# Kernel optimization log

Measured on AMD Instinct MI355X. Metric: run time of the kernel, lower is better.

Reference implementation:

```python
import jax, jax.numpy as jnp
import numpy as np

QMAX = 7.0  # 4-bit symmetric: levels in [-8, 7]

def quant4(w):
    # per-tensor symmetric 4-bit fake-quant with straight-through estimator
    s = jnp.max(jnp.abs(w)) / QMAX
    q = jnp.clip(jnp.round(w / s), -8.0, 7.0) * s
    return w + jax.lax.stop_gradient(q - w)

def setup_inputs() -> dict:
    key = jax.random.key(0)
    ks = jax.random.split(key, 7)
    B = 2048
    x = jax.random.normal(ks[0], (B, 1, 31, 16, 31), dtype=jnp.float32)
    # conv: out_ch=1, in_ch=1, kernel (5,3,5)
    w_conv = jax.random.normal(ks[1], (1, 1, 5, 3, 5), dtype=jnp.float32) * 0.1
    b_conv = jax.random.normal(ks[2], (1,), dtype=jnp.float32) * 0.1
    w_fc1 = jax.random.normal(ks[3], (128, 343), dtype=jnp.float32) * 0.05
    b_fc1 = jax.random.normal(ks[4], (128,), dtype=jnp.float32) * 0.05
    w_fc2 = jax.random.normal(ks[5], (4, 128), dtype=jnp.float32) * 0.05
    b_fc2 = jax.random.normal(ks[6], (4,), dtype=jnp.float32) * 0.05
    return {"x": x, "w_conv": w_conv, "b_conv": b_conv,
            "w_fc1": w_fc1, "b_fc1": b_fc1, "w_fc2": w_fc2, "b_fc2": b_fc2}

def reference(x, w_conv, b_conv, w_fc1, b_fc1, w_fc2, b_fc2):
    # QuantConv3d: 4-bit quantized weights, stride (2,1,2), no padding
    c1 = jax.lax.conv_general_dilated(
        x, quant4(w_conv), window_strides=(2, 1, 2), padding='VALID',
        dimension_numbers=('NCDHW', 'OIDHW', 'NCDHW'))
    c1 = c1 + b_conv.reshape(1, -1, 1, 1, 1)          # [B,1,14,14,14]
    # MaxPool3d(2)
    p1 = jax.lax.reduce_window(c1, -jnp.inf, jax.lax.max,
                               (1, 1, 2, 2, 2), (1, 1, 2, 2, 2), 'VALID')  # [B,1,7,7,7]
    f = p1.reshape(p1.shape[0], -1)                   # [B,343]
    a1 = jax.nn.relu(f @ quant4(w_fc1).T + b_fc1)     # [B,128]
    s2 = a1 @ quant4(w_fc2).T + b_fc2                 # [B,4]
    return jax.nn.softmax(s2, axis=1)
```

## Files before the change

kernel.cpp:

```cpp
#include <hip/hip_runtime.h>

#define WS_WCONV   128
#define WS_W1T     256
#define WS_W2      44160

__device__ __forceinline__ float q4(float w, float s) {
  if (s <= 0.f) return 0.f;
  float r = rintf(w / s);
  r = fminf(fmaxf(r, -8.f), 7.f);
  return r * s;
}

__global__ __launch_bounds__(256) void quant_all(
    const float* __restrict__ wconv, const float* __restrict__ w1,
    const float* __restrict__ w2, float* __restrict__ ws) {
  __shared__ float red[256];
  int b = blockIdx.x, t = threadIdx.x;
  if (b < 88) {
    const float4* w4 = (const float4*)w1;
    float m = 0.f;
    for (int i = t; i < 10976; i += 256) {
      float4 v = w4[i];
      m = fmaxf(m, fmaxf(fmaxf(fabsf(v.x), fabsf(v.y)),
                         fmaxf(fabsf(v.z), fabsf(v.w))));
    }
    red[t] = m;
    __syncthreads();
    for (int s = 128; s > 0; s >>= 1) {
      if (t < s) red[t] = fmaxf(red[t], red[t + s]);
      __syncthreads();
    }
    float s = red[0] * (1.0f / 7.0f);
    #pragma unroll
    for (int k = 0; k < 2; ++k) {
      int idx = b * 512 + k * 256 + t;
      if (idx < 43904) {
        float q = q4(w1[idx], s);
        int o = idx / 343;
        int j = idx - o * 343;
        ws[WS_W1T + j * 128 + o] = q;
      }
    }
  } else {
    float mc = (t < 75) ? fabsf(wconv[t]) : 0.f;
    float m2 = 0.f;
    for (int i = t; i < 512; i += 256) m2 = fmaxf(m2, fabsf(w2[i]));
    red[t] = mc;
    __syncthreads();
    for (int s = 128; s > 0; s >>= 1) {
      if (t < s) red[t] = fmaxf(red[t], red[t + s]);
      __syncthreads();
    }
    float sc = red[0] * (1.0f / 7.0f);
    __syncthreads();
    red[t] = m2;
    __syncthreads();
    for (int s = 128; s > 0; s >>= 1) {
      if (t < s) red[t] = fmaxf(red[t], red[t + s]);
      __syncthreads();
    }
    float s2 = red[0] * (1.0f / 7.0f);
    if (t < 75) ws[WS_WCONV + t] = q4(wconv[t], sc);
    #pragma unroll
    for (int k = 0; k < 2; ++k) {
      int idx = k * 256 + t;
      ws[WS_W2 + idx] = q4(w2[idx], s2);
    }
  }
}

struct __align__(4) f4u { float x, y, z, w; };

__device__ __forceinline__ void conv_global(
    const float* __restrict__ xb, const float* __restrict__ wq,
    int t, float bc, float* __restrict__ feat) {
  if (t >= 343) return;
  int pdl = t / 49;
  int rr  = t - pdl * 49;
  int ph  = rr / 7;
  int pw  = rr - ph * 7;
  float c[2][2][2];
  #pragma unroll
  for (int i = 0; i < 8; ++i) ((float*)c)[i] = 0.f;
  const float* b0 = xb + pdl * 1984 + ph * 62 + pw * 4;
  #pragma unroll
  for (int dd = 0; dd < 7; ++dd) {
    const float* rb = b0 + dd * 496;
    #pragma unroll
    for (int hh = 0; hh < 4; ++hh) {
      const float* rp = rb + hh * 31;
      f4u A = *(const f4u*)rp;
      f4u B = *(const f4u*)(rp + 3);
      float row[7] = {A.x, A.y, A.z, A.w, B.y, B.z, B.w};
      #pragma unroll
      for (int odp = 0; odp < 2; ++odp) {
        int kd = dd - 2 * odp;
        if (kd < 0 || kd > 4) continue;
        #pragma unroll
        for (int ohp = 0; ohp < 2; ++ohp) {
          int kh = hh - ohp;
          if (kh < 0 || kh > 2) continue;
          #pragma unroll
          for (int owp = 0; owp < 2; ++owp) {
            float a = c[odp][ohp][owp];
            #pragma unroll
            for (int kw = 0; kw < 5; ++kw)
              a = fmaf(row[2 * owp + kw], wq[kd * 15 + kh * 5 + kw], a);
            c[odp][ohp][owp] = a;
          }
        }
      }
    }
  }
  float m = ((float*)c)[0];
  #pragma unroll
  for (int i = 1; i < 8; ++i) m = fmaxf(m, ((float*)c)[i]);
  feat[pdl * 49 + rr] = m + bc;
}

__global__ __launch_bounds__(384, 6) void fused_net(
    const float* __restrict__ x, const float* __restrict__ bconv,
    const float* __restrict__ ws, const float* __restrict__ bfc1,
    const float* __restrict__ bfc2, float* __restrict__ out) {
  __shared__ alignas(16) float feat[344];
  __shared__ alignas(16) float fc1p[128];
  __shared__ alignas(16) float a1[128];
  __shared__ float s2[4];
  int t = threadIdx.x;
  int b = blockIdx.x;
  const float* wq = ws + WS_WCONV;
  float bc = bconv[0];
  const float* xb = x + (size_t)b * 15376;

  if (t == 383) feat[343] = 0.f;
  conv_global(xb, wq, t, bc, feat);
  __syncthreads();

  int g = (t >> 7) & 1, o = t & 127;
  float acc = 0.f;
  if (t < 256) {
    const float* w1T = ws + WS_W1T;
    int j0 = g ? 172 : 0;
    const float4* f4 = (const float4*)&feat[j0];
    const float* wp = w1T + j0 * 128 + o;
    float q0 = 0.f, q1 = 0.f, q2 = 0.f, q3 = 0.f;
    for (int q = 0; q < 43; ++q) {
      float4 ff = f4[q];
      q0 = fmaf(ff.x, wp[0],   q0);
      q1 = fmaf(ff.y, wp[128], q1);
      q2 = fmaf(ff.z, wp[256], q2);
      q3 = fmaf(ff.w, wp[384], q3);
      wp += 512;
    }
    acc = (q0 + q1) + (q2 + q3);
    if (g) fc1p[o] = acc;
  }
  __syncthreads();
  if (t < 256 && !g) a1[o] = fmaxf(acc + fc1p[o] + bfc1[o], 0.f);
  __syncthreads();

  if (t < 64) {
    int cls = t & 3, kk = t >> 2;
    const float* w2p = ws + WS_W2 + cls * 128 + kk * 8;
    const float* av = a1 + kk * 8;
    float p = 0.f;
    #pragma unroll
    for (int i = 0; i < 8; ++i) p = fmaf(av[i], w2p[i], p);
    p += __shfl_down(p, 32);
    p += __shfl_down(p, 16);
    p += __shfl_down(p, 8);
    p += __shfl_down(p, 4);
    if (t < 4) s2[t] = p + bfc2[t];
  }
  __syncthreads();
  if (t < 4) {
    float v0 = s2[0], v1 = s2[1], v2 = s2[2], v3 = s2[3];
    float m = fmaxf(fmaxf(v0, v1), fmaxf(v2, v3));
    float e0 = expf(v0 - m), e1 = expf(v1 - m);
    float e2 = expf(v2 - m), e3 = expf(v3 - m);
    float inv = 1.f / (e0 + e1 + e2 + e3);
    float mine = (t == 0) ? e0 : (t == 1) ? e1 : (t == 2) ? e2 : e3;
    out[b * 4 + t] = mine * inv;
  }
}

extern "C" void kernel_launch(void* const* d_in, const int* in_sizes, int n_in,
                              void* d_out, int out_size, void* d_ws, size_t ws_size,
                              hipStream_t stream) {
  const float* x     = (const float*)d_in[0];
  const float* wconv = (const float*)d_in[1];
  const float* bconv = (const float*)d_in[2];
  const float* wfc1  = (const float*)d_in[3];
  const float* bfc1  = (const float*)d_in[4];
  const float* wfc2  = (const float*)d_in[5];
  const float* bfc2  = (const float*)d_in[6];
  float* out = (float*)d_out;
  float* ws  = (float*)d_ws;

  quant_all<<<89, 256, 0, stream>>>(wconv, wfc1, wfc2, ws);
  fused_net<<<2048, 384, 0, stream>>>(x, bconv, ws, bfc1, bfc2, out);
}
```

Measured before the change: 243.4 us.

## Split fused net into dense conv-pool kernel and batched FC kernel

Splits the single fused per-sample kernel into a conv+pool kernel that maps every pooled output across all batches onto fully occupied 256-thread blocks, and an FC kernel that handles four samples per block so each fc1 weight load is reused across four samples. Pooled features go through a workspace buffer in global memory. This removes the idle threads of the 384-thread blocks (only 343 did conv work) and amortizes weight reads. In exchange it adds a global round-trip for features and an extra kernel launch.

```diff
diff --git a/kernel.cpp b/kernel.cpp
--- a/kernel.cpp
+++ b/kernel.cpp
@@ -3,6 +3,7 @@
 #define WS_WCONV   128
 #define WS_W1T     256
 #define WS_W2      44160
+#define WS_FEAT    45056
 
 __device__ __forceinline__ float q4(float w, float s) {
   if (s <= 0.f) return 0.f;
@@ -71,14 +72,19 @@
 
 struct __align__(4) f4u { float x, y, z, w; };
 
-__device__ __forceinline__ void conv_global(
-    const float* __restrict__ xb, const float* __restrict__ wq,
-    int t, float bc, float* __restrict__ feat) {
-  if (t >= 343) return;
-  int pdl = t / 49;
-  int rr  = t - pdl * 49;
-  int ph  = rr / 7;
-  int pw  = rr - ph * 7;
+__global__ __launch_bounds__(256, 8) void conv_pool(
+    const float* __restrict__ x, const float* __restrict__ bconv,
+    const float* __restrict__ ws, float* __restrict__ feat_g) {
+  int gid = blockIdx.x * 256 + threadIdx.x;
+  int batch = (int)(((unsigned long long)(unsigned)gid * 12521772ull) >> 32);
+  int rr = gid - batch * 343;
+  int pdl = (rr * 1338) >> 16;
+  int r2  = rr - pdl * 49;
+  int ph  = (r2 * 9363) >> 16;
+  int pw  = r2 - ph * 7;
+  const float* wq = ws + WS_WCONV;
+  float bc = bconv[0];
+  const float* xb = x + (size_t)batch * 15376;
   float c[2][2][2];
   #pragma unroll
   for (int i = 0; i < 8; ++i) ((float*)c)[i] = 0.f;
@@ -115,54 +121,64 @@
   float m = ((float*)c)[0];
   #pragma unroll
   for (int i = 1; i < 8; ++i) m = fmaxf(m, ((float*)c)[i]);
-  feat[pdl * 49 + rr] = m + bc;
-}
-
-__global__ __launch_bounds__(384, 6) void fused_net(
-    const float* __restrict__ x, const float* __restrict__ bconv,
+  feat_g[(size_t)batch * 344 + rr] = m + bc;
+  if (rr == 0) feat_g[(size_t)batch * 344 + 343] = 0.f;
+}
+
+__global__ __launch_bounds__(256) void fc_net(
     const float* __restrict__ ws, const float* __restrict__ bfc1,
     const float* __restrict__ bfc2, float* __restrict__ out) {
-  __shared__ alignas(16) float feat[344];
-  __shared__ alignas(16) float fc1p[128];
-  __shared__ alignas(16) float a1[128];
-  __shared__ float s2[4];
+  __shared__ alignas(16) float feat[4][344];
+  __shared__ float fc1p[4][128];
+  __shared__ float a1[4][128];
+  __shared__ float s2[4][4];
   int t = threadIdx.x;
-  int b = blockIdx.x;
-  const float* wq = ws + WS_WCONV;
-  float bc = bconv[0];
-  const float* xb = x + (size_t)b * 15376;
-
-  if (t == 383) feat[343] = 0.f;
-  conv_global(xb, wq, t, bc, feat);
+  int b0 = blockIdx.x * 4;
+
+  {
+    const float4* src = (const float4*)(ws + WS_FEAT + (size_t)b0 * 344);
+    float4* dst = (float4*)&feat[0][0];
+    for (int i = t; i < 344; i += 256) dst[i] = src[i];
+  }
   __syncthreads();
 
-  int g = (t >> 7) & 1, o = t & 127;
-  float acc = 0.f;
-  if (t < 256) {
-    const float* w1T = ws + WS_W1T;
+  int g = t >> 7, o = t & 127;
+  {
+    const float* wp = ws + WS_W1T + (g ? 172 * 128 : 0) + o;
     int j0 = g ? 172 : 0;
-    const float4* f4 = (const float4*)&feat[j0];
-    const float* wp = w1T + j0 * 128 + o;
-    float q0 = 0.f, q1 = 0.f, q2 = 0.f, q3 = 0.f;
-    for (int q = 0; q < 43; ++q) {
-      float4 ff = f4[q];
-      q0 = fmaf(ff.x, wp[0],   q0);
-      q1 = fmaf(ff.y, wp[128], q1);
-      q2 = fmaf(ff.z, wp[256], q2);
-      q3 = fmaf(ff.w, wp[384], q3);
+    float q0[4], q1[4], q2[4], q3[4];
+    #pragma unroll
+    for (int bb = 0; bb < 4; ++bb) { q0[bb] = q1[bb] = q2[bb] = q3[bb] = 0.f; }
+    for (int k = 0; k < 43; ++k) {
+      float w0 = wp[0], w1 = wp[128], w2 = wp[256], w3 = wp[384];
+      #pragma unroll
+      for (int bb = 0; bb < 4; ++bb) {
+        float4 ff = *(const float4*)&feat[bb][j0 + k * 4];
+        q0[bb] = fmaf(ff.x, w0, q0[bb]);
+        q1[bb] = fmaf(ff.y, w1, q1[bb]);
+        q2[bb] = fmaf(ff.z, w2, q2[bb]);
+        q3[bb] = fmaf(ff.w, w3, q3[bb]);
+      }
       wp += 512;
     }
-    acc = (q0 + q1) + (q2 + q3);
-    if (g) fc1p[o] = acc;
+    #pragma unroll
+    for (int bb = 0; bb < 4; ++bb) {
+      float acc = (q0[bb] + q1[bb]) + (q2[bb] + q3[bb]);
+      if (g) fc1p[bb][o] = acc;
+      else   a1[bb][o] = acc;
+    }
+    __syncthreads();
+    #pragma unroll
+    for (int bb = 0; bb < 4; ++bb)
+      if (!g) a1[bb][o] = fmaxf(a1[bb][o] + fc1p[bb][o] + bfc1[o], 0.f);
   }
   __syncthreads();
-  if (t < 256 && !g) a1[o] = fmaxf(acc + fc1p[o] + bfc1[o], 0.f);
-  __syncthreads();
-
-  if (t < 64) {
-    int cls = t & 3, kk = t >> 2;
+
+  {
+    int w = t >> 6, l = t & 63;
+    int cls = l & 3, kk = l >> 2;
     const float* w2p = ws + WS_W2 + cls * 128 + kk * 8;
-    const float* av = a1 + kk * 8;
+    const float* av = &a1[w][kk * 8];
     float p = 0.f;
     #pragma unroll
     for (int i = 0; i < 8; ++i) p = fmaf(av[i], w2p[i], p);
@@ -170,17 +186,18 @@
     p += __shfl_down(p, 16);
     p += __shfl_down(p, 8);
     p += __shfl_down(p, 4);
-    if (t < 4) s2[t] = p + bfc2[t];
+    if (l < 4) s2[w][l] = p + bfc2[l];
   }
   __syncthreads();
-  if (t < 4) {
-    float v0 = s2[0], v1 = s2[1], v2 = s2[2], v3 = s2[3];
+  if (t < 16) {
+    int w = t >> 2, cls = t & 3;
+    float v0 = s2[w][0], v1 = s2[w][1], v2 = s2[w][2], v3 = s2[w][3];
     float m = fmaxf(fmaxf(v0, v1), fmaxf(v2, v3));
     float e0 = expf(v0 - m), e1 = expf(v1 - m);
     float e2 = expf(v2 - m), e3 = expf(v3 - m);
     float inv = 1.f / (e0 + e1 + e2 + e3);
-    float mine = (t == 0) ? e0 : (t == 1) ? e1 : (t == 2) ? e2 : e3;
-    out[b * 4 + t] = mine * inv;
+    float mine = (cls == 0) ? e0 : (cls == 1) ? e1 : (cls == 2) ? e2 : e3;
+    out[(b0 + w) * 4 + cls] = mine * inv;
   }
 }
 
@@ -198,5 +215,6 @@
   float* ws  = (float*)d_ws;
 
   quant_all<<<89, 256, 0, stream>>>(wconv, wfc1, wfc2, ws);
-  fused_net<<<2048, 384, 0, stream>>>(x, bconv, ws, bfc1, bfc2, out);
-}
+  conv_pool<<<2744, 256, 0, stream>>>(x, bconv, ws, ws + WS_FEAT);
+  fc_net<<<512, 256, 0, stream>>>(ws, bfc1, bfc2, out);
+}
```

After: 231.7 us. 1.05x faster.
